# Performance work log

Measured on AMD Instinct MI355X. Metric: run time of the kernel, lower is better.

The kernel has to match this reference:

```python
import jax, jax.numpy as jnp
import numpy as np

B, IMG, P, D, E, K, H = 32, 224, 16, 512, 8, 2, 8
G = IMG // P
T = G * G          # 196 patches
PD = P * P         # 256 patch dim
FF = 4 * D         # expert hidden

def _posenc(t, d):
    pos = jnp.arange(t, dtype=jnp.float32)[:, None]
    i = jnp.arange(0, d, 2, dtype=jnp.float32)
    ang = pos / jnp.power(10000.0, i / d)
    pe = jnp.zeros((t, d), jnp.float32)
    pe = pe.at[:, 0::2].set(jnp.sin(ang))
    pe = pe.at[:, 1::2].set(jnp.cos(ang))
    return pe

def _attn(x, Wq, Wk, Wv, Wo, bo):
    bs, t, d = x.shape
    hs = d // H
    q = (x @ Wq).reshape(bs, t, H, hs).transpose(0, 2, 1, 3)
    k = (x @ Wk).reshape(bs, t, H, hs).transpose(0, 2, 1, 3)
    v = (x @ Wv).reshape(bs, t, H, hs).transpose(0, 2, 1, 3)
    wei = jnp.einsum('bhqd,bhkd->bhqk', q, k) * (hs ** -0.5)
    mask = jnp.tril(jnp.ones((t, t), dtype=bool))
    wei = jax.nn.softmax(jnp.where(mask, wei, -jnp.inf), axis=-1)
    o = jnp.einsum('bhqk,bhkd->bhqd', wei, v).transpose(0, 2, 1, 3).reshape(bs, t, d)
    return o @ Wo + bo

def _router(x, Wt, bt, Wn, bn, noise):
    # NoisyTopkRouter: noisy logits, top-k scatter to -inf background, softmax
    logits = x @ Wt + bt
    noisy = logits + noise * jax.nn.softplus(x @ Wn + bn)
    _, topi = jax.lax.top_k(noisy, K)
    sel = jax.nn.one_hot(topi, E, dtype=jnp.float32).sum(-2) > 0  # [B,T,E] bool
    return jax.nn.softmax(jnp.where(sel, noisy, -jnp.inf), axis=-1)

def _moe(x, gate, Wi, bi, Wo, bo):
    # gate is exactly zero off the top-k set, so dense all-expert compute
    # weighted by gate equals the original masked gather/scatter-add combine.
    h = jax.nn.relu(jnp.einsum('btd,edh->bteh', x, Wi) + bi)
    y = jnp.einsum('bteh,ehd->bted', h, Wo) + bo
    return jnp.einsum('bte,bted->btd', gate, y)

def _ln(x, g, b):
    mu = x.mean(-1, keepdims=True)
    var = ((x - mu) ** 2).mean(-1, keepdims=True)
    return (x - mu) / jnp.sqrt(var + 1e-5) * g + b

def _moe_layer(x, pW, pb, Wq, Wk, Wv, Wo, bo, rtW, rtb, rnW, rnb, eWi, ebi, eWo, ebo, lng, lnb, noise):
    x = x @ pW + pb                       # input_projection
    x = _attn(x, Wq, Wk, Wv, Wo, bo)      # multi-head causal self-attention
    gate = _router(x, rtW, rtb, rnW, rnb, noise)
    y = _moe(x, gate, eWi, ebi, eWo, ebo)
    return _ln(y, lng, lnb)               # dropout is identity in eval

def setup_inputs():
    key = jax.random.key(0)
    shapes = {"x": (B, 1, IMG, IMG), "pemb_W": (PD, D), "pemb_b": (D,), "vec_W": (D, D), "vec_b": (D,), "cls_W": (D, D), "cls_b": (D,)}
    for l in ("1", "2"):
        shapes.update({f"p{l}_W": (D, D), f"p{l}_b": (D,), f"Wq{l}": (D, D), f"Wk{l}": (D, D), f"Wv{l}": (D, D), f"Wo{l}": (D, D), f"bo{l}": (D,), f"rt{l}_W": (D, E), f"rt{l}_b": (E,), f"rn{l}_W": (D, E), f"rn{l}_b": (E,), f"eWi{l}": (E, D, FF), f"ebi{l}": (E, FF), f"eWo{l}": (E, FF, D), f"ebo{l}": (E, D), f"ln{l}_g": (D,), f"ln{l}_b": (D,), f"noise{l}": (B, T, E)})
    out = {}
    for i, (name, shp) in enumerate(shapes.items()):
        k = jax.random.fold_in(key, i)
        if name.startswith("ln") and name.endswith("_g"):
            out[name] = jnp.ones(shp, jnp.float32)
        else:
            scale = 1.0 if name == "x" or name.startswith("noise") else 0.02
            out[name] = jax.random.normal(k, shp, jnp.float32) * scale
    return out

def reference(x, pemb_W, pemb_b, vec_W, vec_b, cls_W, cls_b, p1_W, p1_b, Wq1, Wk1, Wv1, Wo1, bo1, rt1_W, rt1_b, rn1_W, rn1_b, eWi1, ebi1, eWo1, ebo1, ln1_g, ln1_b, noise1, p2_W, p2_b, Wq2, Wk2, Wv2, Wo2, bo2, rt2_W, rt2_b, rn2_W, rn2_b, eWi2, ebi2, eWo2, ebo2, ln2_g, ln2_b, noise2):
    bs = x.shape[0]
    # patchify (c==1): [B,1,IMG,IMG] -> [B,T,PD]
    patches = x[:, 0].reshape(bs, G, P, G, P).transpose(0, 1, 3, 2, 4).reshape(bs, T, PD)
    h = patches @ pemb_W + pemb_b + _posenc(T, D)[None]
    f1 = _moe_layer(h, p1_W, p1_b, Wq1, Wk1, Wv1, Wo1, bo1, rt1_W, rt1_b, rn1_W, rn1_b, eWi1, ebi1, eWo1, ebo1, ln1_g, ln1_b, noise1)
    first_vector = f1 @ vec_W + vec_b
    f2 = _moe_layer(first_vector, p2_W, p2_b, Wq2, Wk2, Wv2, Wo2, bo2, rt2_W, rt2_b, rn2_W, rn2_b, eWi2, ebi2, eWo2, ebo2, ln2_g, ln2_b, noise2)
    second_vector = f2 @ vec_W + vec_b
    # source bug: second_attn_weights is None; treated as uniform ones ->
    # mean over dim1 of ones is 1, so global = sum over patches.
    global_vector = second_vector.sum(axis=1)
    cls_vector = global_vector @ cls_W + cls_b
    return first_vector, second_vector, global_vector, cls_vector
```

## Files before the change

kernel.cpp:

```cpp
#include <hip/hip_runtime.h>

#define BT 6272
#define TT 196
#define DM 512
#define FFD 2048
#define NE 8
#define ABUF 3211264
#define SLOTS 12544

typedef float f32x4 __attribute__((ext_vector_type(4)));
typedef __bf16 bf16x8 __attribute__((ext_vector_type(8)));

__device__ __forceinline__ ushort f2bf(float f){
  union { float f; unsigned u; } v; v.f = f;
  unsigned u = v.u;
  u += 0x7fffu + ((u >> 16) & 1u);
  return (ushort)(u >> 16);
}
__device__ __forceinline__ float bf2f(ushort u){
  union { unsigned u; float f; } c; c.u = ((unsigned)u) << 16; return c.f;
}
__device__ __forceinline__ void splitbf(float v, ushort& hi, ushort& lo){
  union { float f; unsigned u; } c; c.f = v;
  hi = (ushort)(c.u >> 16);
  union { unsigned u; float f; } hf; hf.u = c.u & 0xffff0000u;
  lo = f2bf(v - hf.f);
}

__global__ void patchify_k(const float* __restrict__ x, ushort* __restrict__ oh, ushort* __restrict__ ol){
  int bt = blockIdx.x;
  int t = bt % TT, b = bt / TT;
  int pd = threadIdx.x;
  int g1 = t / 14, g2 = t % 14, p1 = pd >> 4, p2 = pd & 15;
  int src = (b*224 + g1*16 + p1)*224 + g2*16 + p2;
  float v = x[src];
  ushort hu, lu; splitbf(v, hu, lu);
  oh[(size_t)bt*256 + pd] = hu;
  ol[(size_t)bt*256 + pd] = lu;
}

__global__ void posenc_k(float* __restrict__ pe){
  int t = blockIdx.x, c = threadIdx.x;
  int m2 = c & ~1;
  double ang = (double)t * pow(10000.0, -(double)m2 / 512.0);
  double vv = (c & 1) ? cos(ang) : sin(ang);
  pe[t*DM + c] = (float)vv;
}

__global__ __launch_bounds__(256)
void wsplit_k(const float* __restrict__ src, ushort* __restrict__ dh, ushort* __restrict__ dl,
              int R, int C){
  __shared__ float t[32][33];
  int c0 = blockIdx.x << 5, r0 = blockIdx.y << 5;
  int tx = threadIdx.x & 31, ty = threadIdx.x >> 5;
  #pragma unroll
  for (int i = 0; i < 32; i += 8)
    t[ty+i][tx] = src[(size_t)(r0+ty+i)*C + c0 + tx];
  __syncthreads();
  #pragma unroll
  for (int i = 0; i < 32; i += 8){
    float v = t[tx][ty+i];
    ushort hu, lu; splitbf(v, hu, lu);
    dh[(size_t)(c0+ty+i)*R + r0 + tx] = hu;
    dl[(size_t)(c0+ty+i)*R + r0 + tx] = lu;
  }
}

__global__ __launch_bounds__(256)
void wsplit5_k(const float* __restrict__ s0, const float* __restrict__ s1,
               const float* __restrict__ s2, const float* __restrict__ s3,
               const float* __restrict__ s4,
               ushort* __restrict__ dWdH, ushort* __restrict__ dWdL,
               ushort* __restrict__ dQkvH, ushort* __restrict__ dQkvL,
               ushort* __restrict__ dWoH, ushort* __restrict__ dWoL)
{
  int z = blockIdx.z;
  const float* src = (z==0)? s0 : (z==1)? s1 : (z==2)? s2 : (z==3)? s3 : s4;
  ushort* dh; ushort* dl;
  if (z == 0){ dh = dWdH; dl = dWdL; }
  else if (z == 4){ dh = dWoH; dl = dWoL; }
  else { dh = dQkvH + (size_t)(z-1)*DM*DM; dl = dQkvL + (size_t)(z-1)*DM*DM; }
  __shared__ float t[32][33];
  int c0 = blockIdx.x << 5, r0 = blockIdx.y << 5;
  int tx = threadIdx.x & 31, ty = threadIdx.x >> 5;
  #pragma unroll
  for (int i = 0; i < 32; i += 8)
    t[ty+i][tx] = src[(size_t)(r0+ty+i)*DM + c0 + tx];
  __syncthreads();
  #pragma unroll
  for (int i = 0; i < 32; i += 8){
    float v = t[tx][ty+i];
    ushort hu, lu; splitbf(v, hu, lu);
    dh[(size_t)(c0+ty+i)*DM + r0 + tx] = hu;
    dl[(size_t)(c0+ty+i)*DM + r0 + tx] = lu;
  }
}

__global__ __launch_bounds__(256)
void gemm_s(const ushort* __restrict__ Ah, const ushort* __restrict__ Al,
            const ushort* __restrict__ Bh, const ushort* __restrict__ Bl,
            const float* __restrict__ bias, const float* __restrict__ pe,
            float* __restrict__ Cf, ushort* __restrict__ Ch, ushort* __restrict__ Cl,
            int N, int kld)
{
  __shared__ ushort Ahs[128][40];
  __shared__ ushort Als[128][40];
  __shared__ ushort Bhs[128][40];
  __shared__ ushort Bls[128][40];
  int tid = threadIdx.x;
  int row0 = blockIdx.y << 7, col0 = blockIdx.x << 7;
  int r = tid >> 1, h16 = (tid & 1) << 4;
  int lane = tid & 63, w = tid >> 6;
  int wr = w >> 1, wc = w & 1;
  const ushort* Aph = Ah + (size_t)(row0 + r) * kld + h16;
  const ushort* Apl = Al + (size_t)(row0 + r) * kld + h16;
  const ushort* Bph = Bh + (size_t)(col0 + r) * kld + h16;
  const ushort* Bpl = Bl + (size_t)(col0 + r) * kld + h16;
  uint4 pah0 = *(const uint4*)(Aph);
  uint4 pah1 = *(const uint4*)(Aph + 8);
  uint4 pal0 = *(const uint4*)(Apl);
  uint4 pal1 = *(const uint4*)(Apl + 8);
  uint4 pbh0 = *(const uint4*)(Bph);
  uint4 pbh1 = *(const uint4*)(Bph + 8);
  uint4 pbl0 = *(const uint4*)(Bpl);
  uint4 pbl1 = *(const uint4*)(Bpl + 8);
  f32x4 acc[4][4] = {};
  int fr = lane & 15, ksel = (lane >> 4) << 3;
  for (int k0 = 32; ; k0 += 32){
    __syncthreads();
    *(uint4*)&Ahs[r][h16]   = pah0;
    *(uint4*)&Ahs[r][h16+8] = pah1;
    *(uint4*)&Als[r][h16]   = pal0;
    *(uint4*)&Als[r][h16+8] = pal1;
    *(uint4*)&Bhs[r][h16]   = pbh0;
    *(uint4*)&Bhs[r][h16+8] = pbh1;
    *(uint4*)&Bls[r][h16]   = pbl0;
    *(uint4*)&Bls[r][h16+8] = pbl1;
    __syncthreads();
    if (k0 < kld){
      pah0 = *(const uint4*)(Aph + k0);
      pah1 = *(const uint4*)(Aph + k0 + 8);
      pal0 = *(const uint4*)(Apl + k0);
      pal1 = *(const uint4*)(Apl + k0 + 8);
      pbh0 = *(const uint4*)(Bph + k0);
      pbh1 = *(const uint4*)(Bph + k0 + 8);
      pbl0 = *(const uint4*)(Bpl + k0);
      pbl1 = *(const uint4*)(Bpl + k0 + 8);
    }
    bf16x8 ah[4], al[4];
    #pragma unroll
    for (int i = 0; i < 4; ++i){
      ah[i] = *(const bf16x8*)&Ahs[(wr<<6) + (i<<4) + fr][ksel];
      al[i] = *(const bf16x8*)&Als[(wr<<6) + (i<<4) + fr][ksel];
    }
    #pragma unroll
    for (int j = 0; j < 4; ++j){
      bf16x8 bh = *(const bf16x8*)&Bhs[(wc<<6) + (j<<4) + fr][ksel];
      bf16x8 bl = *(const bf16x8*)&Bls[(wc<<6) + (j<<4) + fr][ksel];
      #pragma unroll
      for (int i = 0; i < 4; ++i){
        acc[i][j] = __builtin_amdgcn_mfma_f32_16x16x32_bf16(ah[i], bh, acc[i][j], 0, 0, 0);
        acc[i][j] = __builtin_amdgcn_mfma_f32_16x16x32_bf16(al[i], bh, acc[i][j], 0, 0, 0);
        acc[i][j] = __builtin_amdgcn_mfma_f32_16x16x32_bf16(ah[i], bl, acc[i][j], 0, 0, 0);
      }
    }
    if (k0 >= kld) break;
  }
  int fq = lane >> 4;
  #pragma unroll
  for (int j = 0; j < 4; ++j){
    int col = col0 + (wc<<6) + (j<<4) + fr;
    float bv = bias ? bias[col] : 0.f;
    #pragma unroll
    for (int i = 0; i < 4; ++i){
      #pragma unroll
      for (int q = 0; q < 4; ++q){
        int rr = row0 + (wr<<6) + (i<<4) + (fq<<2) + q;
        float v = acc[i][j][q] + bv;
        if (pe) v += pe[(size_t)(rr % TT)*DM + col];
        size_t off = (size_t)rr*N + col;
        if (Cf) Cf[off] = v;
        if (Ch){
          ushort hu, lu; splitbf(v, hu, lu);
          Ch[off] = hu; Cl[off] = lu;
        }
      }
    }
  }
}

__global__ __launch_bounds__(256)
void gemm_f32(const float* __restrict__ A, const float* __restrict__ Bw,
              float* __restrict__ C, const float* __restrict__ bias,
              float* __restrict__ obf, int M, int N, int K)
{
  __shared__ float As[16][68];
  __shared__ float Bs[16][68];
  int tid = threadIdx.x;
  int row0 = blockIdx.y << 6, col0 = blockIdx.x << 6;
  int ar = tid >> 2, ak = (tid & 3) << 2;
  int bk = tid >> 4, bn = (tid & 15) << 2;
  int n0 = (tid & 15) << 2, m0 = (tid >> 4) << 2;
  float acc[4][4] = {};
  bool arow_ok = (row0 + ar) < M;
  const float* Aldg = A + (size_t)(row0 + ar) * K + ak;
  const float* Bldg = Bw + (size_t)bk * N + col0 + bn;
  for (int k0 = 0; k0 < K; k0 += 16){
    float4 av = make_float4(0.f,0.f,0.f,0.f);
    if (arow_ok) av = *(const float4*)(Aldg + k0);
    float4 bv = *(const float4*)(Bldg + (size_t)k0 * N);
    __syncthreads();
    As[ak+0][ar]=av.x; As[ak+1][ar]=av.y; As[ak+2][ar]=av.z; As[ak+3][ar]=av.w;
    *(float4*)&Bs[bk][bn] = bv;
    __syncthreads();
    #pragma unroll
    for (int kk = 0; kk < 16; ++kk){
      float4 a = *(const float4*)&As[kk][m0];
      float4 b = *(const float4*)&Bs[kk][n0];
      float aa[4] = {a.x,a.y,a.z,a.w};
      float bb[4] = {b.x,b.y,b.z,b.w};
      #pragma unroll
      for (int i = 0; i < 4; ++i)
        #pragma unroll
        for (int j = 0; j < 4; ++j)
          acc[i][j] += aa[i]*bb[j];
    }
  }
  float4 badd = make_float4(0.f,0.f,0.f,0.f);
  if (bias) badd = *(const float4*)(bias + col0 + n0);
  #pragma unroll
  for (int i = 0; i < 4; ++i){
    int gr = row0 + m0 + i;
    if (gr < M){
      float4 r = make_float4(acc[i][0]+badd.x, acc[i][1]+badd.y, acc[i][2]+badd.z, acc[i][3]+badd.w);
      *(float4*)(C + (size_t)gr*N + col0 + n0) = r;
      if (obf) *(float4*)(obf + (size_t)gr*N + col0 + n0) = r;
    }
  }
}

__global__ __launch_bounds__(256)
void fattn_k(const ushort* __restrict__ Xh, const ushort* __restrict__ Xl,
             ushort* __restrict__ oh, ushort* __restrict__ ol)
{
  __shared__ ushort Kh[64][72], Kl[64][72];
  __shared__ ushort Vth[64][72], Vtl[64][72];
  __shared__ ushort Ph[64][72], Pl[64][72];
  int qt = blockIdx.x, bh = blockIdx.y;
  int b = bh >> 3, h = bh & 7;
  int tid = threadIdx.x;
  int w = tid >> 6, lane = tid & 63;
  int fr = lane & 15, fu = lane >> 4;
  int qrow_f = qt*64 + w*16 + fr;
  int qtok = b*TT + (qrow_f < TT ? qrow_f : TT-1);
  const ushort* qph = Xh + (size_t)qtok*1536 + h*64 + fu*8;
  const ushort* qpl = Xl + (size_t)qtok*1536 + h*64 + fu*8;
  bf16x8 qh0 = *(const bf16x8*)(qph);
  bf16x8 qh1 = *(const bf16x8*)(qph + 32);
  bf16x8 ql0 = *(const bf16x8*)(qpl);
  bf16x8 ql1 = *(const bf16x8*)(qpl + 32);
  f32x4 o_acc[4] = {};
  float m_i[4], l_i[4];
  #pragma unroll
  for (int q = 0; q < 4; ++q){ m_i[q] = -3e38f; l_i[q] = 0.f; }
  int sr = tid >> 2, sc = (tid & 3) << 4;
  int ktiles = qt + 1;
  for (int kt = 0; kt < ktiles; ++kt){
    __syncthreads();
    {
      int jrow = kt*64 + sr;
      int jtok = b*TT + (jrow < TT ? jrow : TT-1);
      const ushort* kph = Xh + (size_t)jtok*1536 + 512 + h*64 + sc;
      const ushort* kpl = Xl + (size_t)jtok*1536 + 512 + h*64 + sc;
      *(uint4*)&Kh[sr][sc]   = *(const uint4*)kph;
      *(uint4*)&Kh[sr][sc+8] = *(const uint4*)(kph + 8);
      *(uint4*)&Kl[sr][sc]   = *(const uint4*)kpl;
      *(uint4*)&Kl[sr][sc+8] = *(const uint4*)(kpl + 8);
      const ushort* vph = Xh + (size_t)jtok*1536 + 1024 + h*64 + sc;
      const ushort* vpl = Xl + (size_t)jtok*1536 + 1024 + h*64 + sc;
      ushort tv[16];
      *(uint4*)&tv[0] = *(const uint4*)vph;
      *(uint4*)&tv[8] = *(const uint4*)(vph + 8);
      #pragma unroll
      for (int t = 0; t < 16; ++t) Vth[sc + t][sr] = tv[t];
      *(uint4*)&tv[0] = *(const uint4*)vpl;
      *(uint4*)&tv[8] = *(const uint4*)(vpl + 8);
      #pragma unroll
      for (int t = 0; t < 16; ++t) Vtl[sc + t][sr] = tv[t];
    }
    __syncthreads();
    f32x4 sacc[4] = {};
    #pragma unroll
    for (int j = 0; j < 4; ++j){
      bf16x8 kh0 = *(const bf16x8*)&Kh[j*16 + fr][fu*8];
      bf16x8 kh1 = *(const bf16x8*)&Kh[j*16 + fr][32 + fu*8];
      bf16x8 kl0 = *(const bf16x8*)&Kl[j*16 + fr][fu*8];
      bf16x8 kl1 = *(const bf16x8*)&Kl[j*16 + fr][32 + fu*8];
      sacc[j] = __builtin_amdgcn_mfma_f32_16x16x32_bf16(qh0, kh0, sacc[j], 0, 0, 0);
      sacc[j] = __builtin_amdgcn_mfma_f32_16x16x32_bf16(ql0, kh0, sacc[j], 0, 0, 0);
      sacc[j] = __builtin_amdgcn_mfma_f32_16x16x32_bf16(qh0, kl0, sacc[j], 0, 0, 0);
      sacc[j] = __builtin_amdgcn_mfma_f32_16x16x32_bf16(qh1, kh1, sacc[j], 0, 0, 0);
      sacc[j] = __builtin_amdgcn_mfma_f32_16x16x32_bf16(ql1, kh1, sacc[j], 0, 0, 0);
      sacc[j] = __builtin_amdgcn_mfma_f32_16x16x32_bf16(qh1, kl1, sacc[j], 0, 0, 0);
    }
    int rbase = qt*64 + w*16 + (fu<<2);
    int cg = kt*64 + fr;
    float p[4][4];
    #pragma unroll
    for (int q = 0; q < 4; ++q){
      int rg = rbase + q;
      float sv[4];
      #pragma unroll
      for (int j = 0; j < 4; ++j){
        int cj = cg + j*16;
        sv[j] = (cj <= rg && cj < TT) ? sacc[j][q]*0.125f : -3e38f;
      }
      float mx = fmaxf(fmaxf(sv[0],sv[1]), fmaxf(sv[2],sv[3]));
      #pragma unroll
      for (int off = 1; off < 16; off <<= 1) mx = fmaxf(mx, __shfl_xor(mx, off, 64));
      float mnew = fmaxf(m_i[q], mx);
      float al = expf(m_i[q] - mnew);
      l_i[q] *= al;
      o_acc[0][q] *= al; o_acc[1][q] *= al; o_acc[2][q] *= al; o_acc[3][q] *= al;
      float ps = 0.f;
      #pragma unroll
      for (int j = 0; j < 4; ++j){ p[q][j] = expf(sv[j] - mnew); ps += p[q][j]; }
      #pragma unroll
      for (int off = 1; off < 16; off <<= 1) ps += __shfl_xor(ps, off, 64);
      l_i[q] += ps;
      m_i[q] = mnew;
    }
    #pragma unroll
    for (int q = 0; q < 4; ++q){
      int pr = w*16 + (fu<<2) + q;
      #pragma unroll
      for (int j = 0; j < 4; ++j){
        ushort hu, lu; splitbf(p[q][j], hu, lu);
        Ph[pr][j*16 + fr] = hu;
        Pl[pr][j*16 + fr] = lu;
      }
    }
    bf16x8 ph0 = *(const bf16x8*)&Ph[w*16 + fr][fu*8];
    bf16x8 ph1 = *(const bf16x8*)&Ph[w*16 + fr][32 + fu*8];
    bf16x8 pl0 = *(const bf16x8*)&Pl[w*16 + fr][fu*8];
    bf16x8 pl1 = *(const bf16x8*)&Pl[w*16 + fr][32 + fu*8];
    #pragma unroll
    for (int jd = 0; jd < 4; ++jd){
      bf16x8 vh0 = *(const bf16x8*)&Vth[jd*16 + fr][fu*8];
      bf16x8 vh1 = *(const bf16x8*)&Vth[jd*16 + fr][32 + fu*8];
      bf16x8 vl0 = *(const bf16x8*)&Vtl[jd*16 + fr][fu*8];
      bf16x8 vl1 = *(const bf16x8*)&Vtl[jd*16 + fr][32 + fu*8];
      o_acc[jd] = __builtin_amdgcn_mfma_f32_16x16x32_bf16(ph0, vh0, o_acc[jd], 0, 0, 0);
      o_acc[jd] = __builtin_amdgcn_mfma_f32_16x16x32_bf16(pl0, vh0, o_acc[jd], 0, 0, 0);
      o_acc[jd] = __builtin_amdgcn_mfma_f32_16x16x32_bf16(ph0, vl0, o_acc[jd], 0, 0, 0);
      o_acc[jd] = __builtin_amdgcn_mfma_f32_16x16x32_bf16(ph1, vh1, o_acc[jd], 0, 0, 0);
      o_acc[jd] = __builtin_amdgcn_mfma_f32_16x16x32_bf16(pl1, vh1, o_acc[jd], 0, 0, 0);
      o_acc[jd] = __builtin_amdgcn_mfma_f32_16x16x32_bf16(ph1, vl1, o_acc[jd], 0, 0, 0);
    }
  }
  #pragma unroll
  for (int q = 0; q < 4; ++q){
    int rg = qt*64 + w*16 + (fu<<2) + q;
    if (rg < TT){
      float inv = 1.f / l_i[q];
      size_t rowoff = (size_t)(b*TT + rg)*DM + h*64 + fr;
      #pragma unroll
      for (int jd = 0; jd < 4; ++jd){
        float v = o_acc[jd][q] * inv;
        ushort hu, lu; splitbf(v, hu, lu);
        oh[rowoff + jd*16] = hu;
        ol[rowoff + jd*16] = lu;
      }
    }
  }
}

__global__ __launch_bounds__(256)
void router2_k(const ushort* __restrict__ Xh, const ushort* __restrict__ Xl,
               const float* __restrict__ rtW, const float* __restrict__ rtb,
               const float* __restrict__ rnW, const float* __restrict__ rnb, const float* __restrict__ nz,
               int* __restrict__ tok_e, float* __restrict__ tok_g)
{
  __shared__ float Wt[8*513];
  __shared__ float Wn[8*513];
  int tid = threadIdx.x;
  for (int i = tid*4; i < DM*8; i += 1024){
    float4 t = *(const float4*)(rtW + i);
    float4 n = *(const float4*)(rnW + i);
    int d = i >> 3, e = i & 7;
    Wt[(e+0)*513 + d] = t.x; Wt[(e+1)*513 + d] = t.y; Wt[(e+2)*513 + d] = t.z; Wt[(e+3)*513 + d] = t.w;
    Wn[(e+0)*513 + d] = n.x; Wn[(e+1)*513 + d] = n.y; Wn[(e+2)*513 + d] = n.z; Wn[(e+3)*513 + d] = n.w;
  }
  __syncthreads();
  int w = tid >> 6, lane = tid & 63;
  int t = (blockIdx.x << 2) + w;
  const ushort* xh = Xh + (size_t)t * DM;
  const ushort* xl = Xl + (size_t)t * DM;
  float at[8] = {}, an[8] = {};
  #pragma unroll
  for (int u = 0; u < 8; ++u){
    int d = (u<<6) + lane;
    float xv = bf2f(xh[d]) + bf2f(xl[d]);
    #pragma unroll
    for (int e = 0; e < 8; ++e){
      at[e] += xv * Wt[e*513 + d];
      an[e] += xv * Wn[e*513 + d];
    }
  }
  #pragma unroll
  for (int off = 32; off; off >>= 1){
    #pragma unroll
    for (int e = 0; e < 8; ++e){
      at[e] += __shfl_xor(at[e], off, 64);
      an[e] += __shfl_xor(an[e], off, 64);
    }
  }
  if (lane == 0){
    float ns[8];
    #pragma unroll
    for (int e = 0; e < 8; ++e){
      float lt = at[e] + rtb[e];
      float ln_ = an[e] + rnb[e];
      float sp = (ln_ > 0.f) ? (ln_ + log1pf(expf(-ln_))) : log1pf(expf(ln_));
      ns[e] = lt + nz[(size_t)t*8 + e] * sp;
    }
    int i1 = 0; float n1 = ns[0];
    #pragma unroll
    for (int e = 1; e < 8; ++e) if (ns[e] > n1){ n1 = ns[e]; i1 = e; }
    int i2 = -1; float n2 = -3e38f;
    #pragma unroll
    for (int e = 0; e < 8; ++e) if (e != i1 && ns[e] > n2){ n2 = ns[e]; i2 = e; }
    float ex = expf(n2 - n1);
    float inv = 1.f / (1.f + ex);
    tok_e[t*2]   = i1; tok_g[t*2]   = inv;
    tok_e[t*2+1] = i2; tok_g[t*2+1] = ex * inv;
  }
}

__global__ __launch_bounds__(1024)
void route_assign_k(const int* __restrict__ tok_e, int* __restrict__ offs_g,
                    int* __restrict__ idx_c, int* __restrict__ tok_slot)
{
  __shared__ int hist[NE];
  __shared__ int cur[NE];
  int tid = threadIdx.x;
  if (tid < NE) hist[tid] = 0;
  __syncthreads();
  for (int i = tid; i < BT*2; i += 1024) atomicAdd(&hist[tok_e[i]], 1);
  __syncthreads();
  if (tid == 0){
    int s = 0;
    for (int e = 0; e < NE; ++e){ offs_g[e] = s; cur[e] = s; s += hist[e]; }
    offs_g[NE] = s;
  }
  __syncthreads();
  for (int i = tid; i < BT*2; i += 1024){
    int e = tok_e[i];
    int p = atomicAdd(&cur[e], 1);
    idx_c[p] = i >> 1;
    tok_slot[i] = p;
  }
}

__global__ __launch_bounds__(256)
void transconv_k(const float* __restrict__ src, ushort* __restrict__ dst, int R, int C){
  __shared__ float t[32][33];
  int e = blockIdx.z;
  src += (size_t)e * R * C;
  dst += (size_t)e * R * C;
  int c0 = blockIdx.x << 5, r0 = blockIdx.y << 5;
  int tx = threadIdx.x & 31, ty = threadIdx.x >> 5;
  #pragma unroll
  for (int i = 0; i < 32; i += 8)
    t[ty+i][tx] = src[(size_t)(r0+ty+i)*C + c0 + tx];
  __syncthreads();
  #pragma unroll
  for (int i = 0; i < 32; i += 8)
    dst[(size_t)(c0+ty+i)*R + r0 + tx] = f2bf(t[tx][ty+i]);
}

__global__ void gatherconv_k(const ushort* __restrict__ Xh, const int* __restrict__ idx,
                             ushort* __restrict__ Xg){
  int s = blockIdx.x;
  const ushort* xp = Xh + (size_t)idx[s] * DM;
  ushort* op = Xg + (size_t)s * DM;
  int i = threadIdx.x * 2;
  *(ushort2*)(op + i) = *(const ushort2*)(xp + i);
}

template<int MODE>
__global__ __launch_bounds__(256)
void moe_mfma(const ushort* __restrict__ A, const ushort* __restrict__ Bt,
              const float* __restrict__ bias, const int* __restrict__ offs,
              void* __restrict__ Out, int kld, int ldb, int out_ld, int accum)
{
  int e = blockIdx.z;
  int base = offs[e], cnt = offs[e+1] - base;
  int row0 = blockIdx.y << 7;
  if (row0 >= cnt) return;
  int col0 = blockIdx.x << 7;
  __shared__ ushort As[128][40];
  __shared__ ushort Bs[128][40];
  int tid = threadIdx.x;
  int r = tid >> 1, h = (tid & 1) << 4;
  int lane = tid & 63, w = tid >> 6;
  int wr = w >> 1, wc = w & 1;
  int sidx = base + row0 + r; if (sidx > SLOTS-1) sidx = SLOTS-1;
  const ushort* Ap = A + (size_t)sidx * kld + h;
  const ushort* Bp = Bt + (size_t)e * ((size_t)FFD*DM) + (size_t)(col0 + r) * ldb + h;
  uint4 pa0 = *(const uint4*)Ap;
  uint4 pa1 = *(const uint4*)(Ap + 8);
  uint4 pb0 = *(const uint4*)Bp;
  uint4 pb1 = *(const uint4*)(Bp + 8);
  f32x4 acc[4][4] = {};
  int fr = lane & 15, ksel = (lane >> 4) << 3;
  int k0 = 0;
  while (true){
    __syncthreads();
    *(uint4*)&As[r][h]     = pa0;
    *(uint4*)&As[r][h + 8] = pa1;
    *(uint4*)&Bs[r][h]     = pb0;
    *(uint4*)&Bs[r][h + 8] = pb1;
    __syncthreads();
    k0 += 32;
    if (k0 < kld){
      pa0 = *(const uint4*)(Ap + k0);
      pa1 = *(const uint4*)(Ap + k0 + 8);
      pb0 = *(const uint4*)(Bp + k0);
      pb1 = *(const uint4*)(Bp + k0 + 8);
    }
    bf16x8 af[4], bf[4];
    #pragma unroll
    for (int i = 0; i < 4; ++i){
      af[i] = *(const bf16x8*)&As[(wr<<6) + (i<<4) + fr][ksel];
      bf[i] = *(const bf16x8*)&Bs[(wc<<6) + (i<<4) + fr][ksel];
    }
    #pragma unroll
    for (int i = 0; i < 4; ++i)
      #pragma unroll
      for (int j = 0; j < 4; ++j)
        acc[i][j] = __builtin_amdgcn_mfma_f32_16x16x32_bf16(af[i], bf[j], acc[i][j], 0, 0, 0);
    if (k0 >= kld) break;
  }
  int fq = lane >> 4;
  #pragma unroll
  for (int j = 0; j < 4; ++j){
    int col = col0 + (wc<<6) + (j<<4) + fr;
    float bv = bias[(size_t)e * ((MODE==0)?FFD:DM) + col];
    #pragma unroll
    for (int i = 0; i < 4; ++i){
      #pragma unroll
      for (int q = 0; q < 4; ++q){
        int rr = row0 + (wr<<6) + (i<<4) + (fq<<2) + q;
        if (rr < cnt){
          if (MODE == 0){
            float vv = acc[i][j][q] + bv;
            ((ushort*)Out)[(size_t)(base+rr)*out_ld + col] = f2bf(fmaxf(vv, 0.f));
          } else {
            float* yp = (float*)Out + (size_t)(base+rr)*out_ld + col;
            *yp = acc[i][j][q] + (accum ? *yp : bv);
          }
        }
      }
    }
  }
}

__global__ __launch_bounds__(256)
void combine_ln_k(const float* __restrict__ Ye, const int* __restrict__ tok_slot,
                  const float* __restrict__ tok_g, const float* __restrict__ g,
                  const float* __restrict__ bb, ushort* __restrict__ oh, ushort* __restrict__ ol)
{
  int t = blockIdx.x, tid = threadIdx.x;
  int s1 = tok_slot[t*2], s2 = tok_slot[t*2+1];
  float g1 = tok_g[t*2], g2 = tok_g[t*2+1];
  const float* y1 = Ye + (size_t)s1*DM;
  const float* y2 = Ye + (size_t)s2*DM;
  float v0 = g1*y1[tid]     + g2*y2[tid];
  float v1 = g1*y1[tid+256] + g2*y2[tid+256];
  __shared__ float red[8];
  int w = tid >> 6, lane = tid & 63;
  float s = v0 + v1;
  #pragma unroll
  for (int off = 32; off; off >>= 1) s += __shfl_xor(s, off, 64);
  if (lane == 0) red[w] = s;
  __syncthreads();
  float mu = (red[0]+red[1]+red[2]+red[3]) * (1.f/512.f);
  float d0 = v0 - mu, d1 = v1 - mu;
  float q2 = d0*d0 + d1*d1;
  #pragma unroll
  for (int off = 32; off; off >>= 1) q2 += __shfl_xor(q2, off, 64);
  if (lane == 0) red[4+w] = q2;
  __syncthreads();
  float var = (red[4]+red[5]+red[6]+red[7]) * (1.f/512.f);
  float r = 1.f / sqrtf(var + 1e-5f);
  float r0v = d0*r*g[tid]     + bb[tid];
  float r1v = d1*r*g[tid+256] + bb[tid+256];
  ushort hu, lu;
  splitbf(r0v, hu, lu);
  oh[(size_t)t*DM + tid] = hu; ol[(size_t)t*DM + tid] = lu;
  splitbf(r1v, hu, lu);
  oh[(size_t)t*DM + tid + 256] = hu; ol[(size_t)t*DM + tid + 256] = lu;
}

__global__ void gsum_k(const float* __restrict__ sv, float* __restrict__ gb, float* __restrict__ gout){
  int i = blockIdx.x*256 + threadIdx.x;
  int b = i >> 9, d = i & 511;
  const float* p = sv + (size_t)b*TT*DM + d;
  float s = 0.f;
  for (int t = 0; t < TT; ++t) s += p[(size_t)t*DM];
  gb[i] = s; gout[i] = s;
}

extern "C" void kernel_launch(void* const* d_in, const int* in_sizes, int n_in,
                              void* d_out, int out_size, void* d_ws, size_t ws_size,
                              hipStream_t stream)
{
  (void)in_sizes; (void)n_in; (void)out_size;
  const float* xin   = (const float*)d_in[0];
  const float* pembW = (const float*)d_in[1];
  const float* pembB = (const float*)d_in[2];
  const float* vecW  = (const float*)d_in[3];
  const float* vecB  = (const float*)d_in[4];
  const float* clsW  = (const float*)d_in[5];
  const float* clsB  = (const float*)d_in[6];
  float* out = (float*)d_out;

  const size_t QKV_SH = (size_t)2 * BT * 1536;
  const size_t BASEF =
      (size_t)SLOTS*DM
    + (size_t)2*ABUF
    + (size_t)SLOTS*DM/2
    + (size_t)NE*FFD*DM
    + (2*256*DM + 2*DM*DM + 2*3*DM*DM + 2*DM*DM + 2*DM*DM)/2
    + (size_t)TT*DM
    + 16384*2 + SLOTS + SLOTS*3 + 64;
  int fcw = 1024;
  for (int cand = 2048; cand >= 256; cand >>= 1){
    size_t reg_sh = (size_t)SLOTS*cand > QKV_SH ? (size_t)SLOTS*cand : QKV_SH;
    size_t need = (BASEF + reg_sh/2) * sizeof(float);
    if (need <= ws_size){ fcw = cand; break; }
  }
  size_t region_sh = (size_t)SLOTS*fcw > QKV_SH ? (size_t)SLOTS*fcw : QKV_SH;

  float* ws = (float*)d_ws;
  float* Yexp = ws;
  ushort* S0h = (ushort*)(Yexp + (size_t)SLOTS*DM);
  ushort* S0l = S0h + ABUF;
  ushort* S1h = S0l + ABUF;
  ushort* S1l = S1h + ABUF;
  ushort* region = S1l + ABUF;
  ushort* Xg   = region + region_sh;
  ushort* WiT  = Xg + (size_t)SLOTS*DM;
  ushort* WoT  = WiT + (size_t)NE*FFD*DM;
  ushort* PembH = WoT + (size_t)NE*FFD*DM;
  ushort* PembL = PembH + 256*DM;
  ushort* VecH = PembL + 256*DM;
  ushort* VecL = VecH + DM*DM;
  ushort* QkvWH = VecL + DM*DM;
  ushort* QkvWL = QkvWH + 3*DM*DM;
  ushort* WoSH = QkvWL + 3*DM*DM;
  ushort* WoSL = WoSH + DM*DM;
  ushort* WdH  = WoSL + DM*DM;
  ushort* WdL  = WdH + DM*DM;
  float* pe    = (float*)(WdL + DM*DM);
  float* gbv   = pe + TT*DM;
  float* clsbuf= gbv + 16384;
  float* tok_g = clsbuf + 16384;
  int* tok_e   = (int*)(tok_g + SLOTS);
  int* tok_slot= tok_e + SLOTS;
  int* idx_c   = tok_slot + SLOTS;
  int* offs    = idx_c + SLOTS;
  ushort* QKVh = region;
  ushort* QKVl = region + (size_t)BT*1536;
  ushort* H1b  = region;
  ushort* PATh = region;
  ushort* PATl = region + (size_t)BT*256;

  patchify_k<<<dim3(BT), dim3(256), 0, stream>>>(xin, PATh, PATl);
  posenc_k<<<dim3(TT), dim3(512), 0, stream>>>(pe);
  wsplit_k<<<dim3(16, 8), dim3(256), 0, stream>>>(pembW, PembH, PembL, 256, DM);
  wsplit_k<<<dim3(16, 16), dim3(256), 0, stream>>>(vecW, VecH, VecL, DM, DM);
  gemm_s<<<dim3(4,49), dim3(256), 0, stream>>>(PATh, PATl, PembH, PembL, pembB, pe,
                                               nullptr, S0h, S0l, DM, 256);

  ushort *INh = S0h, *INl = S0l, *TPh = S1h, *TPl = S1l;
  for (int l = 0; l < 2; ++l){
    int base = 7 + 18*l;
    const float* pW  = (const float*)d_in[base+0];
    const float* pb  = (const float*)d_in[base+1];
    const float* Wq  = (const float*)d_in[base+2];
    const float* Wk  = (const float*)d_in[base+3];
    const float* Wv  = (const float*)d_in[base+4];
    const float* Wo  = (const float*)d_in[base+5];
    const float* bo  = (const float*)d_in[base+6];
    const float* rtW = (const float*)d_in[base+7];
    const float* rtb = (const float*)d_in[base+8];
    const float* rnW = (const float*)d_in[base+9];
    const float* rnb = (const float*)d_in[base+10];
    const float* eWi = (const float*)d_in[base+11];
    const float* ebi = (const float*)d_in[base+12];
    const float* eWo = (const float*)d_in[base+13];
    const float* ebo = (const float*)d_in[base+14];
    const float* lng = (const float*)d_in[base+15];
    const float* lnb = (const float*)d_in[base+16];
    const float* nz  = (const float*)d_in[base+17];

    wsplit5_k<<<dim3(16,16,5), dim3(256), 0, stream>>>(pW, Wq, Wk, Wv, Wo,
                                                       WdH, WdL, QkvWH, QkvWL, WoSH, WoSL);
    gemm_s<<<dim3(4,49), dim3(256), 0, stream>>>(INh, INl, WdH, WdL, pb, nullptr,
                                                 nullptr, TPh, TPl, DM, DM);
    gemm_s<<<dim3(12,49), dim3(256), 0, stream>>>(TPh, TPl, QkvWH, QkvWL, nullptr, nullptr,
                                                 nullptr, QKVh, QKVl, 1536, DM);
    fattn_k<<<dim3(4,256), dim3(256), 0, stream>>>(QKVh, QKVl, INh, INl);
    gemm_s<<<dim3(4,49), dim3(256), 0, stream>>>(INh, INl, WoSH, WoSL, bo, nullptr,
                                                 nullptr, TPh, TPl, DM, DM);
    transconv_k<<<dim3(FFD/32, DM/32, NE), dim3(256), 0, stream>>>(eWi, WiT, DM, FFD);
    transconv_k<<<dim3(DM/32, FFD/32, NE), dim3(256), 0, stream>>>(eWo, WoT, FFD, DM);
    router2_k<<<dim3(BT/4), dim3(256), 0, stream>>>(TPh, TPl, rtW, rtb, rnW, rnb, nz, tok_e, tok_g);
    route_assign_k<<<dim3(1), dim3(1024), 0, stream>>>(tok_e, offs, idx_c, tok_slot);
    gatherconv_k<<<dim3(SLOTS), dim3(256), 0, stream>>>(TPh, idx_c, Xg);
    for (int c0 = 0; c0 < FFD; c0 += fcw){
      moe_mfma<0><<<dim3(fcw/128, 49, NE), dim3(256), 0, stream>>>(
          Xg, WiT + (size_t)c0*DM, ebi + c0, offs, (void*)H1b, DM, DM, fcw, 0);
      moe_mfma<1><<<dim3(DM/128, 49, NE), dim3(256), 0, stream>>>(
          H1b, WoT + c0, ebo, offs, (void*)Yexp, fcw, FFD, DM, c0);
    }
    combine_ln_k<<<dim3(BT), dim3(256), 0, stream>>>(Yexp, tok_slot, tok_g, lng, lnb, INh, INl);
    gemm_s<<<dim3(4,49), dim3(256), 0, stream>>>(INh, INl, VecH, VecL, vecB, nullptr,
                                                 out + (size_t)l*ABUF, TPh, TPl, DM, DM);
    ushort* th = INh; INh = TPh; TPh = th;
    ushort* tl = INl; INl = TPl; TPl = tl;
  }

  gsum_k<<<dim3(64), dim3(256), 0, stream>>>(out + ABUF, gbv, out + 2*ABUF);
  gemm_f32<<<dim3(8,1), dim3(256), 0, stream>>>(gbv, clsW, clsbuf, clsB, out + 2*ABUF + 16384, 32, DM, DM);
}
```

Baseline: 1.067 ms.

## Fold input projection into QKV weights and use direct global-to-LDS loads

Precomputes fused weights (pW @ Wqkv) and a folded bias once per layer, so the separate input-projection GEMM over all tokens is removed and the QKV GEMM reads the layer input directly. Both the split-bf16 GEMM and the MoE GEMM now load tiles with global_load_lds into an unpadded, XOR-swizzled LDS layout instead of register prefetch plus LDS stores. The default expert chunk width drops from 1024 to 256. The GEMM loops lose their register double-buffering, so global load latency may be exposed, and the folded weights add a small rounding difference.

```diff
diff --git a/kernel.cpp b/kernel.cpp
--- a/kernel.cpp
+++ b/kernel.cpp
@@ -25,6 +25,11 @@
   hi = (ushort)(c.u >> 16);
   union { unsigned u; float f; } hf; hf.u = c.u & 0xffff0000u;
   lo = f2bf(v - hf.f);
+}
+__device__ __forceinline__ void glds16(const ushort* g, ushort* l){
+  __builtin_amdgcn_global_load_lds(
+      (const __attribute__((address_space(1))) unsigned int*)g,
+      (__attribute__((address_space(3))) unsigned int*)l, 16, 0, 0);
 }
 
 __global__ void patchify_k(const float* __restrict__ x, ushort* __restrict__ oh, ushort* __restrict__ ol){
@@ -67,19 +72,16 @@
 }
 
 __global__ __launch_bounds__(256)
-void wsplit5_k(const float* __restrict__ s0, const float* __restrict__ s1,
+void wsplit4_k(const float* __restrict__ s0, const float* __restrict__ s1,
                const float* __restrict__ s2, const float* __restrict__ s3,
-               const float* __restrict__ s4,
-               ushort* __restrict__ dWdH, ushort* __restrict__ dWdL,
                ushort* __restrict__ dQkvH, ushort* __restrict__ dQkvL,
                ushort* __restrict__ dWoH, ushort* __restrict__ dWoL)
 {
   int z = blockIdx.z;
-  const float* src = (z==0)? s0 : (z==1)? s1 : (z==2)? s2 : (z==3)? s3 : s4;
+  const float* src = (z==0)? s0 : (z==1)? s1 : (z==2)? s2 : s3;
   ushort* dh; ushort* dl;
-  if (z == 0){ dh = dWdH; dl = dWdL; }
-  else if (z == 4){ dh = dWoH; dl = dWoL; }
-  else { dh = dQkvH + (size_t)(z-1)*DM*DM; dl = dQkvL + (size_t)(z-1)*DM*DM; }
+  if (z == 3){ dh = dWoH; dl = dWoL; }
+  else { dh = dQkvH + (size_t)z*DM*DM; dl = dQkvL + (size_t)z*DM*DM; }
   __shared__ float t[32][33];
   int c0 = blockIdx.x << 5, r0 = blockIdx.y << 5;
   int tx = threadIdx.x & 31, ty = threadIdx.x >> 5;
@@ -96,6 +98,28 @@
   }
 }
 
+__global__ void esplit_k(const float* __restrict__ src, ushort* __restrict__ dh, ushort* __restrict__ dl){
+  int i = blockIdx.x*256 + threadIdx.x;
+  ushort hu, lu; splitbf(src[i], hu, lu);
+  dh[i] = hu; dl[i] = lu;
+}
+
+__global__ __launch_bounds__(256)
+void bfold_k(const float* __restrict__ pb, const float* __restrict__ Wq,
+             const float* __restrict__ Wk, const float* __restrict__ Wv,
+             float* __restrict__ bf){
+  __shared__ float pbs[DM];
+  int tid = threadIdx.x;
+  for (int i = tid; i < DM; i += 256) pbs[i] = pb[i];
+  __syncthreads();
+  int n = blockIdx.x*256 + tid;
+  const float* W = (n < 512) ? Wq : (n < 1024) ? Wk : Wv;
+  int c = n & 511;
+  float s = 0.f;
+  for (int d = 0; d < DM; ++d) s += pbs[d] * W[(size_t)d*DM + c];
+  bf[n] = s;
+}
+
 __global__ __launch_bounds__(256)
 void gemm_s(const ushort* __restrict__ Ah, const ushort* __restrict__ Al,
             const ushort* __restrict__ Bh, const ushort* __restrict__ Bl,
@@ -103,60 +127,51 @@
             float* __restrict__ Cf, ushort* __restrict__ Ch, ushort* __restrict__ Cl,
             int N, int kld)
 {
-  __shared__ ushort Ahs[128][40];
-  __shared__ ushort Als[128][40];
-  __shared__ ushort Bhs[128][40];
-  __shared__ ushort Bls[128][40];
+  __shared__ ushort Ahs[128*32];
+  __shared__ ushort Als[128*32];
+  __shared__ ushort Bhs[128*32];
+  __shared__ ushort Bls[128*32];
   int tid = threadIdx.x;
   int row0 = blockIdx.y << 7, col0 = blockIdx.x << 7;
-  int r = tid >> 1, h16 = (tid & 1) << 4;
   int lane = tid & 63, w = tid >> 6;
   int wr = w >> 1, wc = w & 1;
-  const ushort* Aph = Ah + (size_t)(row0 + r) * kld + h16;
-  const ushort* Apl = Al + (size_t)(row0 + r) * kld + h16;
-  const ushort* Bph = Bh + (size_t)(col0 + r) * kld + h16;
-  const ushort* Bpl = Bl + (size_t)(col0 + r) * kld + h16;
-  uint4 pah0 = *(const uint4*)(Aph);
-  uint4 pah1 = *(const uint4*)(Aph + 8);
-  uint4 pal0 = *(const uint4*)(Apl);
-  uint4 pal1 = *(const uint4*)(Apl + 8);
-  uint4 pbh0 = *(const uint4*)(Bph);
-  uint4 pbh1 = *(const uint4*)(Bph + 8);
-  uint4 pbl0 = *(const uint4*)(Bpl);
-  uint4 pbl1 = *(const uint4*)(Bpl + 8);
+  int fr = lane & 15, fu = lane >> 4;
+  int srow = 16*w + (lane >> 2);
+  int cs = ((lane & 3) ^ ((srow >> 1) & 3)) << 3;
+  const ushort* gAh0 = Ah + (size_t)(row0 + srow) * kld + cs;
+  const ushort* gAh1 = Ah + (size_t)(row0 + 64 + srow) * kld + cs;
+  const ushort* gAl0 = Al + (size_t)(row0 + srow) * kld + cs;
+  const ushort* gAl1 = Al + (size_t)(row0 + 64 + srow) * kld + cs;
+  const ushort* gBh0 = Bh + (size_t)(col0 + srow) * kld + cs;
+  const ushort* gBh1 = Bh + (size_t)(col0 + 64 + srow) * kld + cs;
+  const ushort* gBl0 = Bl + (size_t)(col0 + srow) * kld + cs;
+  const ushort* gBl1 = Bl + (size_t)(col0 + 64 + srow) * kld + cs;
+  ushort* lAh0 = &Ahs[(16*w)*32];      ushort* lAh1 = &Ahs[(64+16*w)*32];
+  ushort* lAl0 = &Als[(16*w)*32];      ushort* lAl1 = &Als[(64+16*w)*32];
+  ushort* lBh0 = &Bhs[(16*w)*32];      ushort* lBh1 = &Bhs[(64+16*w)*32];
+  ushort* lBl0 = &Bls[(16*w)*32];      ushort* lBl1 = &Bls[(64+16*w)*32];
   f32x4 acc[4][4] = {};
-  int fr = lane & 15, ksel = (lane >> 4) << 3;
-  for (int k0 = 32; ; k0 += 32){
+  for (int k0 = 0; k0 < kld; k0 += 32){
     __syncthreads();
-    *(uint4*)&Ahs[r][h16]   = pah0;
-    *(uint4*)&Ahs[r][h16+8] = pah1;
-    *(uint4*)&Als[r][h16]   = pal0;
-    *(uint4*)&Als[r][h16+8] = pal1;
-    *(uint4*)&Bhs[r][h16]   = pbh0;
-    *(uint4*)&Bhs[r][h16+8] = pbh1;
-    *(uint4*)&Bls[r][h16]   = pbl0;
-    *(uint4*)&Bls[r][h16+8] = pbl1;
+    glds16(gAh0 + k0, lAh0); glds16(gAh1 + k0, lAh1);
+    glds16(gAl0 + k0, lAl0); glds16(gAl1 + k0, lAl1);
+    glds16(gBh0 + k0, lBh0); glds16(gBh1 + k0, lBh1);
+    glds16(gBl0 + k0, lBl0); glds16(gBl1 + k0, lBl1);
     __syncthreads();
-    if (k0 < kld){
-      pah0 = *(const uint4*)(Aph + k0);
-      pah1 = *(const uint4*)(Aph + k0 + 8);
-      pal0 = *(const uint4*)(Apl + k0);
-      pal1 = *(const uint4*)(Apl + k0 + 8);
-      pbh0 = *(const uint4*)(Bph + k0);
-      pbh1 = *(const uint4*)(Bph + k0 + 8);
-      pbl0 = *(const uint4*)(Bpl + k0);
-      pbl1 = *(const uint4*)(Bpl + k0 + 8);
-    }
     bf16x8 ah[4], al[4];
     #pragma unroll
     for (int i = 0; i < 4; ++i){
-      ah[i] = *(const bf16x8*)&Ahs[(wr<<6) + (i<<4) + fr][ksel];
-      al[i] = *(const bf16x8*)&Als[(wr<<6) + (i<<4) + fr][ksel];
+      int Ra = (wr<<6) + (i<<4) + fr;
+      int oa = Ra*32 + ((fu ^ ((Ra>>1)&3))<<3);
+      ah[i] = *(const bf16x8*)&Ahs[oa];
+      al[i] = *(const bf16x8*)&Als[oa];
     }
     #pragma unroll
     for (int j = 0; j < 4; ++j){
-      bf16x8 bh = *(const bf16x8*)&Bhs[(wc<<6) + (j<<4) + fr][ksel];
-      bf16x8 bl = *(const bf16x8*)&Bls[(wc<<6) + (j<<4) + fr][ksel];
+      int Rb = (wc<<6) + (j<<4) + fr;
+      int ob = Rb*32 + ((fu ^ ((Rb>>1)&3))<<3);
+      bf16x8 bh = *(const bf16x8*)&Bhs[ob];
+      bf16x8 bl = *(const bf16x8*)&Bls[ob];
       #pragma unroll
       for (int i = 0; i < 4; ++i){
         acc[i][j] = __builtin_amdgcn_mfma_f32_16x16x32_bf16(ah[i], bh, acc[i][j], 0, 0, 0);
@@ -164,7 +179,6 @@
         acc[i][j] = __builtin_amdgcn_mfma_f32_16x16x32_bf16(ah[i], bl, acc[i][j], 0, 0, 0);
       }
     }
-    if (k0 >= kld) break;
   }
   int fq = lane >> 4;
   #pragma unroll
@@ -499,48 +513,43 @@
   int row0 = blockIdx.y << 7;
   if (row0 >= cnt) return;
   int col0 = blockIdx.x << 7;
-  __shared__ ushort As[128][40];
-  __shared__ ushort Bs[128][40];
-  int tid = threadIdx.x;
-  int r = tid >> 1, h = (tid & 1) << 4;
-  int lane = tid & 63, w = tid >> 6;
+  __shared__ ushort As[128*32];
+  __shared__ ushort Bs[128*32];
+  int tid = threadIdx.x, lane = tid & 63, w = tid >> 6;
   int wr = w >> 1, wc = w & 1;
-  int sidx = base + row0 + r; if (sidx > SLOTS-1) sidx = SLOTS-1;
-  const ushort* Ap = A + (size_t)sidx * kld + h;
-  const ushort* Bp = Bt + (size_t)e * ((size_t)FFD*DM) + (size_t)(col0 + r) * ldb + h;
-  uint4 pa0 = *(const uint4*)Ap;
-  uint4 pa1 = *(const uint4*)(Ap + 8);
-  uint4 pb0 = *(const uint4*)Bp;
-  uint4 pb1 = *(const uint4*)(Bp + 8);
+  int fr = lane & 15, fu = lane >> 4;
+  int srow = 16*w + (lane >> 2);
+  int cs = ((lane & 3) ^ ((srow >> 1) & 3)) << 3;
+  int ar0 = base + row0 + srow;      if (ar0 > SLOTS-1) ar0 = SLOTS-1;
+  int ar1 = base + row0 + 64 + srow; if (ar1 > SLOTS-1) ar1 = SLOTS-1;
+  const ushort* gA0 = A + (size_t)ar0 * kld + cs;
+  const ushort* gA1 = A + (size_t)ar1 * kld + cs;
+  const ushort* Bb = Bt + (size_t)e * ((size_t)FFD*DM);
+  const ushort* gB0 = Bb + (size_t)(col0 + srow) * ldb + cs;
+  const ushort* gB1 = Bb + (size_t)(col0 + 64 + srow) * ldb + cs;
+  ushort* lA0 = &As[(16*w)*32];  ushort* lA1 = &As[(64+16*w)*32];
+  ushort* lB0 = &Bs[(16*w)*32];  ushort* lB1 = &Bs[(64+16*w)*32];
   f32x4 acc[4][4] = {};
-  int fr = lane & 15, ksel = (lane >> 4) << 3;
-  int k0 = 0;
-  while (true){
+  for (int k0 = 0; k0 < kld; k0 += 32){
     __syncthreads();
-    *(uint4*)&As[r][h]     = pa0;
-    *(uint4*)&As[r][h + 8] = pa1;
-    *(uint4*)&Bs[r][h]     = pb0;
-    *(uint4*)&Bs[r][h + 8] = pb1;
+    glds16(gA0 + k0, lA0);
+    glds16(gA1 + k0, lA1);
+    glds16(gB0 + k0, lB0);
+    glds16(gB1 + k0, lB1);
     __syncthreads();
-    k0 += 32;
-    if (k0 < kld){
-      pa0 = *(const uint4*)(Ap + k0);
-      pa1 = *(const uint4*)(Ap + k0 + 8);
-      pb0 = *(const uint4*)(Bp + k0);
-      pb1 = *(const uint4*)(Bp + k0 + 8);
-    }
     bf16x8 af[4], bf[4];
     #pragma unroll
     for (int i = 0; i < 4; ++i){
-      af[i] = *(const bf16x8*)&As[(wr<<6) + (i<<4) + fr][ksel];
-      bf[i] = *(const bf16x8*)&Bs[(wc<<6) + (i<<4) + fr][ksel];
+      int Ra = (wr<<6) + (i<<4) + fr;
+      af[i] = *(const bf16x8*)&As[Ra*32 + ((fu ^ ((Ra>>1)&3))<<3)];
+      int Rb = (wc<<6) + (i<<4) + fr;
+      bf[i] = *(const bf16x8*)&Bs[Rb*32 + ((fu ^ ((Rb>>1)&3))<<3)];
     }
     #pragma unroll
     for (int i = 0; i < 4; ++i)
       #pragma unroll
       for (int j = 0; j < 4; ++j)
         acc[i][j] = __builtin_amdgcn_mfma_f32_16x16x32_bf16(af[i], bf[j], acc[i][j], 0, 0, 0);
-    if (k0 >= kld) break;
   }
   int fq = lane >> 4;
   #pragma unroll
@@ -626,22 +635,26 @@
   const float* clsB  = (const float*)d_in[6];
   float* out = (float*)d_out;
 
-  const size_t QKV_SH = (size_t)2 * BT * 1536;
-  const size_t BASEF =
+  const size_t QKV_SH  = (size_t)2*BT*1536;
+  const size_t RMIN_SH = QKV_SH + (size_t)2*1536*DM + (size_t)2*DM*DM;
+  const size_t FIXF =
       (size_t)SLOTS*DM
     + (size_t)2*ABUF
     + (size_t)SLOTS*DM/2
     + (size_t)NE*FFD*DM
-    + (2*256*DM + 2*DM*DM + 2*3*DM*DM + 2*DM*DM + 2*DM*DM)/2
-    + (size_t)TT*DM
+    + (size_t)256*DM
+    + (size_t)DM*DM
+    + (size_t)3*DM*DM
+    + (size_t)DM*DM
+    + (size_t)TT*DM + 2048
     + 16384*2 + SLOTS + SLOTS*3 + 64;
-  int fcw = 1024;
+  int fcw = 256;
   for (int cand = 2048; cand >= 256; cand >>= 1){
-    size_t reg_sh = (size_t)SLOTS*cand > QKV_SH ? (size_t)SLOTS*cand : QKV_SH;
-    size_t need = (BASEF + reg_sh/2) * sizeof(float);
+    size_t reg_sh = (size_t)SLOTS*cand > RMIN_SH ? (size_t)SLOTS*cand : RMIN_SH;
+    size_t need = (FIXF + reg_sh/2) * sizeof(float);
     if (need <= ws_size){ fcw = cand; break; }
   }
-  size_t region_sh = (size_t)SLOTS*fcw > QKV_SH ? (size_t)SLOTS*fcw : QKV_SH;
+  size_t region_sh = (size_t)SLOTS*fcw > RMIN_SH ? (size_t)SLOTS*fcw : RMIN_SH;
 
   float* ws = (float*)d_ws;
   float* Yexp = ws;
@@ -661,10 +674,9 @@
   ushort* QkvWL = QkvWH + 3*DM*DM;
   ushort* WoSH = QkvWL + 3*DM*DM;
   ushort* WoSL = WoSH + DM*DM;
-  ushort* WdH  = WoSL + DM*DM;
-  ushort* WdL  = WdH + DM*DM;
-  float* pe    = (float*)(WdL + DM*DM);
-  float* gbv   = pe + TT*DM;
+  float* pe    = (float*)(WoSL + DM*DM);
+  float* bfold = pe + TT*DM;
+  float* gbv   = bfold + 2048;
   float* clsbuf= gbv + 16384;
   float* tok_g = clsbuf + 16384;
   int* tok_e   = (int*)(tok_g + SLOTS);
@@ -673,6 +685,10 @@
   int* offs    = idx_c + SLOTS;
   ushort* QKVh = region;
   ushort* QKVl = region + (size_t)BT*1536;
+  ushort* FoldWH = region + QKV_SH;
+  ushort* FoldWL = FoldWH + (size_t)1536*DM;
+  ushort* PWh  = FoldWL + (size_t)1536*DM;
+  ushort* PWl  = PWh + (size_t)DM*DM;
   ushort* H1b  = region;
   ushort* PATh = region;
   ushort* PATl = region + (size_t)BT*256;
@@ -706,11 +722,13 @@
     const float* lnb = (const float*)d_in[base+16];
     const float* nz  = (const float*)d_in[base+17];
 
-    wsplit5_k<<<dim3(16,16,5), dim3(256), 0, stream>>>(pW, Wq, Wk, Wv, Wo,
-                                                       WdH, WdL, QkvWH, QkvWL, WoSH, WoSL);
-    gemm_s<<<dim3(4,49), dim3(256), 0, stream>>>(INh, INl, WdH, WdL, pb, nullptr,
-                                                 nullptr, TPh, TPl, DM, DM);
-    gemm_s<<<dim3(12,49), dim3(256), 0, stream>>>(TPh, TPl, QkvWH, QkvWL, nullptr, nullptr,
+    wsplit4_k<<<dim3(16,16,4), dim3(256), 0, stream>>>(Wq, Wk, Wv, Wo,
+                                                       QkvWH, QkvWL, WoSH, WoSL);
+    esplit_k<<<dim3(1024), dim3(256), 0, stream>>>(pW, PWh, PWl);
+    gemm_s<<<dim3(4,12), dim3(256), 0, stream>>>(QkvWH, QkvWL, PWh, PWl, nullptr, nullptr,
+                                                 nullptr, FoldWH, FoldWL, DM, DM);
+    bfold_k<<<dim3(6), dim3(256), 0, stream>>>(pb, Wq, Wk, Wv, bfold);
+    gemm_s<<<dim3(12,49), dim3(256), 0, stream>>>(INh, INl, FoldWH, FoldWL, bfold, nullptr,
                                                  nullptr, QKVh, QKVl, 1536, DM);
     fattn_k<<<dim3(4,256), dim3(256), 0, stream>>>(QKVh, QKVl, INh, INl);
     gemm_s<<<dim3(4,49), dim3(256), 0, stream>>>(INh, INl, WoSH, WoSL, bo, nullptr,
```

After: 1.141 ms. +7.0%, slower.
